# Performance work log

Measured on AMD Instinct MI355X. Metric: run time of the kernel, lower is better.

The kernel has to match this reference:

```python
import jax, jax.numpy as jnp
import numpy as np

WINDOW = 30     # sliding_window_size
STRIDE = 2      # unfold stride
TOP_K = 3       # top_k_chunks


def setup_inputs() -> dict:
    key = jax.random.key(0)
    ks = jax.random.split(key, 10)
    B, Q, D, E = 8, 30, 1500, 768
    mu = jnp.array([1.0, 0.9, 0.7, 0.5, 0.3, 0.1, -0.1, -0.3, -0.5, -0.7, -0.9], jnp.float32)
    sigma = jnp.array([0.001] + [0.1] * 10, jnp.float32)
    u = lambda k, s: jax.random.uniform(k, s, jnp.float32, -0.014, 0.014)
    return {
        'query_embeddings': jax.random.normal(ks[0], (B, Q, E), jnp.float32),
        'document_embeddings': jax.random.normal(ks[1], (B, D, E), jnp.float32),
        'query_pad_oov_mask': jnp.ones((B, Q), jnp.float32),
        'document_pad_oov_mask': jnp.ones((B, D), jnp.float32),
        'query_idfs': jax.random.uniform(ks[2], (B, Q, 1), jnp.float32),
        'document_idfs': jax.random.uniform(ks[3], (B, D, 1), jnp.float32),
        'mu': mu,
        'sigma': sigma,
        'sat_w1': u(ks[4], (1, 2)), 'sat_b1': jnp.full((1,), 100.0, jnp.float32),
        'sat_w2': u(ks[5], (1, 2)), 'sat_b2': jnp.full((1,), 100.0, jnp.float32),
        'sat_w3': u(ks[6], (1, 2)), 'sat_b3': jnp.full((1,), 100.0, jnp.float32),
        'dense_w': u(ks[7], (1, 11)),
        'chunk_scoring': jnp.ones((1, TOP_K * 5), jnp.float32),
    }


def _skl_forward(q_emb, d_emb, q_mask, d_mask, q_idfs,
                 mu, sigma, sat_w1, sat_b1, sat_w2, sat_b2, sat_w3, sat_b3,
                 dense_w, chunk_scoring):
    B, Qn, E = q_emb.shape
    D = d_emb.shape[1]
    # cosine similarity matrix [B, Q, D]
    qn = q_emb / jnp.clip(jnp.linalg.norm(q_emb, axis=-1, keepdims=True), 1e-13)
    dn = d_emb / jnp.clip(jnp.linalg.norm(d_emb, axis=-1, keepdims=True), 1e-13)
    cos = jnp.einsum('bqe,bde->bqd', qn, dn)
    # RBF kernel bank [B, Q, D, K]
    rk = jnp.exp(-(cos[..., None] - mu) ** 2 / (2.0 * sigma ** 2))
    km = rk * d_mask[:, None, :, None]
    # sliding-window unfold over doc dim: [B, Q, W, WINDOW, K]
    W = (D - WINDOW) // STRIDE + 1
    win_idx = jnp.arange(W)[:, None] * STRIDE + jnp.arange(WINDOW)[None, :]
    unr = km[:, :, win_idx, :]
    lengths = jnp.sum(jnp.sum(unr, -1) != 0, -1)            # [B, Q, W]
    pkq = jnp.sum(unr, -2)                                   # [B, Q, W, K]
    # idf saturation branch
    idf = jnp.broadcast_to(jax.nn.relu(q_idfs), (B, Qn, W))[..., None]
    infl = jnp.concatenate([idf, lengths.astype(jnp.float32)[..., None]], -1)  # [B,Q,W,2]
    sat1 = infl @ sat_w1.T + sat_b1
    sat2 = 1.0 / (infl @ sat_w2.T + sat_b2)
    sat3 = infl @ sat_w3.T + sat_b3
    spkq = sat1 * jnp.clip(pkq, 1e-10) ** sat2 - sat3
    spkq = spkq * q_mask[:, :, None, None] * (lengths > 0).astype(jnp.float32)[..., None]
    per_kernel = jnp.sum(spkq, 1)                            # [B, W, K]
    score = (per_kernel @ dense_w.T)[..., 0]                 # [B, W]
    s0 = jnp.where(score == 0, -9900.0, score)
    # greedy non-overlapping top-k chunk selection
    mprs = s0
    r = jnp.arange(W)
    best_idx = []
    for c in range(TOP_K):
        best = jnp.argmax(mprs, axis=1)                      # [B]
        best_idx.append(best)
        pool = jnp.abs(r[None, :] - best[:, None]) < (WINDOW / 2)
        mprs = jnp.where(pool, -10001.0 - c, mprs)
    top_idx = jnp.stack(best_idx, axis=1)                    # [B, TOP_K]
    nb = jnp.concatenate([top_idx, top_idx - 1, top_idx + 1,
                          top_idx - 2, top_idx + 2], axis=1)
    nb = jnp.clip(nb, 0, W - 1)
    topk = jnp.take_along_axis(s0, nb, axis=1)               # [B, TOP_K*5]
    topk = jnp.where(topk <= -9900.0, 0.0, topk)
    return jnp.sum(topk * chunk_scoring, axis=1)             # [B]


def reference(query_embeddings, document_embeddings, query_pad_oov_mask,
              document_pad_oov_mask, query_idfs, document_idfs,
              mu, sigma, sat_w1, sat_b1, sat_w2, sat_b2, sat_w3, sat_b3,
              dense_w, chunk_scoring):
    return _skl_forward(query_embeddings, document_embeddings,
                        query_pad_oov_mask, document_pad_oov_mask, query_idfs,
                        mu, sigma, sat_w1, sat_b1, sat_w2, sat_b2,
                        sat_w3, sat_b3, dense_w, chunk_scoring)
```

## Files before the change

### kernel.cpp

```cpp
#include <hip/hip_runtime.h>

#define BB 8
#define QQ 30
#define DD 1500
#define EE 768
#define KK 11
#define WW 736
#define WIN 30
#define STR 2

#define NT 94
#define DCH 544

typedef __attribute__((ext_vector_type(8))) __bf16 bf16x8;
typedef __attribute__((ext_vector_type(4))) float f32x4;
typedef __attribute__((ext_vector_type(4))) unsigned int uint4v;

__device__ inline void split8(const float4 va, const float4 vb,
                              bf16x8& bh, bf16x8& bl, float& ssq)
{
    float f[8] = {va.x, va.y, va.z, va.w, vb.x, vb.y, vb.z, vb.w};
    unsigned hu[8];
    float r[8];
    #pragma unroll
    for (int j = 0; j < 8; j++) {
        float x = f[j];
        ssq += x * x;
        unsigned hb = __float_as_uint(x) & 0xffff0000u;
        hu[j] = hb;
        r[j] = x - __uint_as_float(hb);
    }
    uint4v uh, ul;
    #pragma unroll
    for (int j = 0; j < 4; j++) {
        uh[j] = hu[2 * j + 1] | (hu[2 * j] >> 16);
        unsigned l0 = __float_as_uint(r[2 * j]) >> 16;
        unsigned l1 = __float_as_uint(r[2 * j + 1]) & 0xffff0000u;
        ul[j] = l1 | l0;
    }
    bh = __builtin_bit_cast(bf16x8, uh);
    bl = __builtin_bit_cast(bf16x8, ul);
}

#define MFMA(a, b, c) __builtin_amdgcn_mfma_f32_16x16x32_bf16(a, b, c, 0, 0, 0)

__global__ __launch_bounds__(256) void skl_gemm(
    const float* __restrict__ qe,
    const float* __restrict__ de,
    float* __restrict__ cosm)
{
    __shared__ float red[4][64][12];
    __shared__ float qinv[32];
    int tid = threadIdx.x;
    int wave = tid >> 6, lane = tid & 63;
    int ln = lane & 15, g = lane >> 4;
    int nt = blockIdx.x, b = blockIdx.y;
    int d = nt * 16 + ln;
    int dc = min(d, DD - 1);
    const float* drow  = de + ((size_t)b * DD + dc) * EE;
    int r1 = min(16 + ln, QQ - 1);
    const float* qrow0 = qe + ((size_t)b * QQ + ln) * EE;
    const float* qrow1 = qe + ((size_t)b * QQ + r1) * EE;

    f32x4 acc0 = {0.f, 0.f, 0.f, 0.f};
    f32x4 acc1 = {0.f, 0.f, 0.f, 0.f};
    float dssq = 0.f, qssq0 = 0.f, qssq1 = 0.f;
    int k0 = wave * 192;

    #pragma unroll
    for (int kst = 0; kst < 6; kst++) {
        int e0 = k0 + kst * 32 + 8 * g;
        bf16x8 a0h, a0l, a1h, a1l, bh, bl;
        {
            float4 va = *(const float4*)&qrow0[e0];
            float4 vb = *(const float4*)&qrow0[e0 + 4];
            split8(va, vb, a0h, a0l, qssq0);
        }
        {
            float4 va = *(const float4*)&qrow1[e0];
            float4 vb = *(const float4*)&qrow1[e0 + 4];
            split8(va, vb, a1h, a1l, qssq1);
        }
        {
            float4 va = *(const float4*)&drow[e0];
            float4 vb = *(const float4*)&drow[e0 + 4];
            split8(va, vb, bh, bl, dssq);
        }
        acc0 = MFMA(a0h, bh, acc0);
        acc0 = MFMA(a0h, bl, acc0);
        acc0 = MFMA(a0l, bh, acc0);
        acc1 = MFMA(a1h, bh, acc1);
        acc1 = MFMA(a1h, bl, acc1);
        acc1 = MFMA(a1l, bh, acc1);
    }

    dssq  += __shfl_xor(dssq, 16);  dssq  += __shfl_xor(dssq, 32);
    qssq0 += __shfl_xor(qssq0, 16); qssq0 += __shfl_xor(qssq0, 32);
    qssq1 += __shfl_xor(qssq1, 16); qssq1 += __shfl_xor(qssq1, 32);

    #pragma unroll
    for (int j = 0; j < 4; j++) {
        red[wave][lane][j] = acc0[j];
        red[wave][lane][4 + j] = acc1[j];
    }
    red[wave][lane][8] = dssq;
    red[wave][lane][9] = qssq0;
    red[wave][lane][10] = qssq1;
    __syncthreads();

    if (tid < 16) {
        float q0 = 0.f, q1 = 0.f;
        #pragma unroll
        for (int w = 0; w < 4; w++) {
            q0 += red[w][tid][9];
            q1 += red[w][tid][10];
        }
        qinv[tid]      = 1.f / fmaxf(sqrtf(q0), 1e-13f);
        qinv[16 + tid] = 1.f / fmaxf(sqrtf(q1), 1e-13f);
    }
    __syncthreads();

    if (wave == 0) {
        float a0f[4] = {0.f, 0.f, 0.f, 0.f};
        float a1f[4] = {0.f, 0.f, 0.f, 0.f};
        float sf = 0.f;
        #pragma unroll
        for (int w = 0; w < 4; w++) {
            #pragma unroll
            for (int j = 0; j < 4; j++) {
                a0f[j] += red[w][lane][j];
                a1f[j] += red[w][lane][4 + j];
            }
            sf += red[w][lane][8];
        }
        float dinv = 1.f / fmaxf(sqrtf(sf), 1e-13f);
        if (d < DD) {
            #pragma unroll
            for (int j = 0; j < 4; j++) {
                int q0 = 4 * g + j;
                cosm[((size_t)b * QQ + q0) * DD + d] = a0f[j] * dinv * qinv[q0];
                int q1i = 16 + q0;
                if (q1i < QQ)
                    cosm[((size_t)b * QQ + q1i) * DD + d] = a1f[j] * dinv * qinv[q1i];
            }
        }
    }
}

__global__ __launch_bounds__(256) void skl_windows(
    const float* __restrict__ cosm,
    const float* __restrict__ dmask,
    const float* __restrict__ qmask,
    const float* __restrict__ qidfs,
    const float* __restrict__ mu,
    const float* __restrict__ sigma,
    const float* __restrict__ w1, const float* __restrict__ b1,
    const float* __restrict__ w2, const float* __restrict__ b2,
    const float* __restrict__ w3, const float* __restrict__ b3,
    const float* __restrict__ dw,
    float* __restrict__ pscore)
{
    __shared__ float vf[KK][DCH];
    __shared__ float fl[DCH];

    int bid = blockIdx.x;
    int c  = bid % 3;
    int bq = bid / 3;
    int b  = bq / QQ;
    int tid = threadIdx.x;

    int dbase = 512 * c;
    int dcount = min(540, DD - dbase);
    int w = c * 256 + tid;
    bool active = (w < WW);

    float muL[KK], i2s[KK], dwL[KK];
    #pragma unroll
    for (int k = 0; k < KK; k++) {
        muL[k] = mu[k];
        float s = sigma[k];
        i2s[k] = 1.f / (2.f * s * s);
        dwL[k] = dw[k];
    }
    const float* dm = dmask + (size_t)b * DD + dbase;
    const float* crow = cosm + (size_t)bq * DD + dbase;

    for (int i = tid; i < dcount; i += 256) {
        float cc = crow[i];
        float m = dm[i];
        float ssum = 0.f;
        #pragma unroll
        for (int k = 0; k < KK; k++) {
            float diff = cc - muL[k];
            float val = __expf(-diff * diff * i2s[k]) * m;
            ssum += val;
            vf[k][i] = val;
        }
        fl[i] = (ssum != 0.f) ? 1.f : 0.f;
    }
    __syncthreads();

    if (active) {
        int dl = 2 * tid;
        float pk[KK];
        #pragma unroll
        for (int k = 0; k < KK; k++) pk[k] = 0.f;
        float lenf = 0.f;
        #pragma unroll
        for (int j2 = 0; j2 < WIN / 2; j2++) {
            float2 f2 = *(const float2*)&fl[dl + 2 * j2];
            lenf += f2.x + f2.y;
            #pragma unroll
            for (int k = 0; k < KK; k++) {
                float2 v2 = *(const float2*)&vf[k][dl + 2 * j2];
                pk[k] += v2.x + v2.y;
            }
        }
        float idf = fmaxf(qidfs[bq], 0.f);
        float sat1 = idf * w1[0] + lenf * w1[1] + b1[0];
        float sat2 = 1.f / (idf * w2[0] + lenf * w2[1] + b2[0]);
        float sat3 = idf * w3[0] + lenf * w3[1] + b3[0];
        float mult = qmask[bq] * (lenf > 0.f ? 1.f : 0.f);

        float acc = 0.f;
        #pragma unroll
        for (int k = 0; k < KK; k++) {
            float x = fmaxf(pk[k], 1e-10f);
            float p = exp2f(sat2 * __log2f(x));
            acc += (sat1 * p - sat3) * dwL[k];
        }
        pscore[(size_t)bq * WW + w] = acc * mult;
    }
}

__global__ __launch_bounds__(256) void skl_topk(
    const float* __restrict__ pscore,
    const float* __restrict__ chunk,
    float* __restrict__ out)
{
    __shared__ float s0[WW];
    int b = blockIdx.x;
    int tid = threadIdx.x;

    if (tid < WW / 4) {
        float4 s = make_float4(0.f, 0.f, 0.f, 0.f);
        for (int q = 0; q < QQ; q++) {
            float4 v = *(const float4*)&pscore[(size_t)(b * QQ + q) * WW + 4 * tid];
            s.x += v.x; s.y += v.y; s.z += v.z; s.w += v.w;
        }
        s0[4 * tid + 0] = (s.x == 0.f) ? -9900.f : s.x;
        s0[4 * tid + 1] = (s.y == 0.f) ? -9900.f : s.y;
        s0[4 * tid + 2] = (s.z == 0.f) ? -9900.f : s.z;
        s0[4 * tid + 3] = (s.w == 0.f) ? -9900.f : s.w;
    }
    __syncthreads();

    if (tid < 64) {
        int lane = tid;
        float m[12];
        #pragma unroll
        for (int r = 0; r < 12; r++) {
            int w = lane + 64 * r;
            m[r] = (w < WW) ? s0[w] : -3.3e38f;
        }

        int best[3];
        for (int c = 0; c < 3; c++) {
            float bv = -3.3e38f;
            int bi = 1 << 30;
            #pragma unroll
            for (int r = 0; r < 12; r++) {
                int w = lane + 64 * r;
                if (w < WW && m[r] > bv) { bv = m[r]; bi = w; }
            }
            #pragma unroll
            for (int off = 32; off >= 1; off >>= 1) {
                float ov = __shfl_down(bv, off);
                int oi = __shfl_down(bi, off);
                if (ov > bv || (ov == bv && oi < bi)) { bv = ov; bi = oi; }
            }
            bi = __shfl(bi, 0);
            best[c] = bi;
            float pen = -10001.f - (float)c;
            #pragma unroll
            for (int r = 0; r < 12; r++) {
                int w = lane + 64 * r;
                int dd = w - bi; if (dd < 0) dd = -dd;
                if (w < WW && dd < 15) m[r] = pen;
            }
        }

        float contrib = 0.f;
        if (lane < 15) {
            int c = lane % 3;
            int g = lane / 3;
            const int offs[5] = {0, -1, 1, -2, 2};
            int nb = best[c] + offs[g];
            nb = min(max(nb, 0), WW - 1);
            float v = s0[nb];
            if (v <= -9900.f) v = 0.f;
            contrib = v * chunk[lane];
        }
        #pragma unroll
        for (int off = 32; off >= 1; off >>= 1) contrib += __shfl_down(contrib, off);
        if (lane == 0) out[b] = contrib;
    }
}

extern "C" void kernel_launch(void* const* d_in, const int* in_sizes, int n_in,
                              void* d_out, int out_size, void* d_ws, size_t ws_size,
                              hipStream_t stream) {
    const float* qe    = (const float*)d_in[0];
    const float* de    = (const float*)d_in[1];
    const float* qmask = (const float*)d_in[2];
    const float* dmask = (const float*)d_in[3];
    const float* qidfs = (const float*)d_in[4];
    const float* mu    = (const float*)d_in[6];
    const float* sigma = (const float*)d_in[7];
    const float* w1    = (const float*)d_in[8];
    const float* b1    = (const float*)d_in[9];
    const float* w2    = (const float*)d_in[10];
    const float* b2    = (const float*)d_in[11];
    const float* w3    = (const float*)d_in[12];
    const float* b3    = (const float*)d_in[13];
    const float* dw    = (const float*)d_in[14];
    const float* chunk = (const float*)d_in[15];
    float* out = (float*)d_out;

    float* ws = (float*)d_ws;
    float* cosm   = ws;
    float* pscore = ws + 360000;

    skl_gemm<<<dim3(NT, BB), 256, 0, stream>>>(qe, de, cosm);
    skl_windows<<<BB * QQ * 3, 256, 0, stream>>>(cosm, dmask, qmask, qidfs,
                                                 mu, sigma, w1, b1, w2, b2, w3, b3,
                                                 dw, pscore);
    skl_topk<<<BB, 256, 0, stream>>>(pscore, chunk, out);
}
```

Baseline: 33.94 us.

## Split GEMM reduction dimension across two blocks and finish normalization in window kernel

```diff
diff --git a/kernel.cpp b/kernel.cpp
--- a/kernel.cpp
+++ b/kernel.cpp
@@ -10,6 +10,7 @@
 #define STR 2
 
 #define NT 94
+#define KS 2
 #define DCH 544
 
 typedef __attribute__((ext_vector_type(8))) __bf16 bf16x8;
@@ -47,14 +48,15 @@
 __global__ __launch_bounds__(256) void skl_gemm(
     const float* __restrict__ qe,
     const float* __restrict__ de,
-    float* __restrict__ cosm)
+    float* __restrict__ cpart,
+    float* __restrict__ dssqp,
+    float* __restrict__ qssqp)
 {
     __shared__ float red[4][64][12];
-    __shared__ float qinv[32];
     int tid = threadIdx.x;
     int wave = tid >> 6, lane = tid & 63;
     int ln = lane & 15, g = lane >> 4;
-    int nt = blockIdx.x, b = blockIdx.y;
+    int nt = blockIdx.x, ks = blockIdx.y, b = blockIdx.z;
     int d = nt * 16 + ln;
     int dc = min(d, DD - 1);
     const float* drow  = de + ((size_t)b * DD + dc) * EE;
@@ -65,10 +67,10 @@
     f32x4 acc0 = {0.f, 0.f, 0.f, 0.f};
     f32x4 acc1 = {0.f, 0.f, 0.f, 0.f};
     float dssq = 0.f, qssq0 = 0.f, qssq1 = 0.f;
-    int k0 = wave * 192;
-
-    #pragma unroll
-    for (int kst = 0; kst < 6; kst++) {
+    int k0 = ks * 384 + wave * 96;
+
+    #pragma unroll
+    for (int kst = 0; kst < 3; kst++) {
         int e0 = k0 + kst * 32 + 8 * g;
         bf16x8 a0h, a0l, a1h, a1l, bh, bl;
         {
@@ -115,10 +117,9 @@
             q0 += red[w][tid][9];
             q1 += red[w][tid][10];
         }
-        qinv[tid]      = 1.f / fmaxf(sqrtf(q0), 1e-13f);
-        qinv[16 + tid] = 1.f / fmaxf(sqrtf(q1), 1e-13f);
-    }
-    __syncthreads();
+        qssqp[ks * (BB * QQ) + b * QQ + tid] = q0;
+        if (16 + tid < QQ) qssqp[ks * (BB * QQ) + b * QQ + 16 + tid] = q1;
+    }
 
     if (wave == 0) {
         float a0f[4] = {0.f, 0.f, 0.f, 0.f};
@@ -133,22 +134,25 @@
             }
             sf += red[w][lane][8];
         }
-        float dinv = 1.f / fmaxf(sqrtf(sf), 1e-13f);
         if (d < DD) {
+            size_t sbase = (size_t)ks * (BB * QQ) * DD;
             #pragma unroll
             for (int j = 0; j < 4; j++) {
                 int q0 = 4 * g + j;
-                cosm[((size_t)b * QQ + q0) * DD + d] = a0f[j] * dinv * qinv[q0];
+                cpart[sbase + ((size_t)b * QQ + q0) * DD + d] = a0f[j];
                 int q1i = 16 + q0;
                 if (q1i < QQ)
-                    cosm[((size_t)b * QQ + q1i) * DD + d] = a1f[j] * dinv * qinv[q1i];
-            }
+                    cpart[sbase + ((size_t)b * QQ + q1i) * DD + d] = a1f[j];
+            }
+            dssqp[((size_t)ks * BB + b) * DD + d] = sf;
         }
     }
 }
 
 __global__ __launch_bounds__(256) void skl_windows(
-    const float* __restrict__ cosm,
+    const float* __restrict__ cpart,
+    const float* __restrict__ dssqp,
+    const float* __restrict__ qssqp,
     const float* __restrict__ dmask,
     const float* __restrict__ qmask,
     const float* __restrict__ qidfs,
@@ -183,10 +187,17 @@
         dwL[k] = dw[k];
     }
     const float* dm = dmask + (size_t)b * DD + dbase;
-    const float* crow = cosm + (size_t)bq * DD + dbase;
+    const float* c0 = cpart + (size_t)bq * DD + dbase;
+    const float* c1 = c0 + (size_t)(BB * QQ) * DD;
+    const float* s0p = dssqp + (size_t)b * DD + dbase;
+    const float* s1p = s0p + (size_t)BB * DD;
+    float qin = 1.f / fmaxf(sqrtf(qssqp[bq] + qssqp[BB * QQ + bq]), 1e-13f);
 
     for (int i = tid; i < dcount; i += 256) {
-        float cc = crow[i];
+        float dot = c0[i] + c1[i];
+        float dsq = s0p[i] + s1p[i];
+        float invd = 1.f / fmaxf(sqrtf(dsq), 1e-13f);
+        float cc = dot * invd * qin;
         float m = dm[i];
         float ssum = 0.f;
         #pragma unroll
@@ -328,12 +339,15 @@
     float* out = (float*)d_out;
 
     float* ws = (float*)d_ws;
-    float* cosm   = ws;
-    float* pscore = ws + 360000;
-
-    skl_gemm<<<dim3(NT, BB), 256, 0, stream>>>(qe, de, cosm);
-    skl_windows<<<BB * QQ * 3, 256, 0, stream>>>(cosm, dmask, qmask, qidfs,
-                                                 mu, sigma, w1, b1, w2, b2, w3, b3,
+    float* cpart  = ws;
+    float* dssqp  = ws + 720000;
+    float* qssqp  = ws + 744000;
+    float* pscore = ws + 744512;
+
+    skl_gemm<<<dim3(NT, KS, BB), 256, 0, stream>>>(qe, de, cpart, dssqp, qssqp);
+    skl_windows<<<BB * QQ * 3, 256, 0, stream>>>(cpart, dssqp, qssqp, dmask,
+                                                 qmask, qidfs, mu, sigma,
+                                                 w1, b1, w2, b2, w3, b3,
                                                  dw, pscore);
     skl_topk<<<BB, 256, 0, stream>>>(pscore, chunk, out);
 }
```

Result: slower. 36.04 us (+6.2%).
